# Kernel tuning notes

Hardware: AMD Instinct MI355X
Metric: run time of the kernel (lower is better)

The kernel has to match this reference:

```python
import jax, jax.numpy as jnp
import numpy as np

PATCH = 8      # patch_size
NFREQ = 8      # fourie_freq


def _fourier_feats(nH, nW, F, dtype):
    # Per-patch positional Fourier features: sin/cos of normalized patch-center
    # coords at F dyadic frequencies for both axes -> [nH, nW, 4F].
    iy = (jnp.arange(nH, dtype=jnp.float32) + 0.5) / nH
    ix = (jnp.arange(nW, dtype=jnp.float32) + 0.5) / nW
    freqs = (2.0 ** jnp.arange(F, dtype=jnp.float32)) * jnp.pi
    fy = iy[:, None] * freqs[None, :]  # [nH, F]
    fx = ix[:, None] * freqs[None, :]  # [nW, F]
    feats = jnp.concatenate([
        jnp.broadcast_to(jnp.sin(fy)[:, None, :], (nH, nW, F)),
        jnp.broadcast_to(jnp.cos(fy)[:, None, :], (nH, nW, F)),
        jnp.broadcast_to(jnp.sin(fx)[None, :, :], (nH, nW, F)),
        jnp.broadcast_to(jnp.cos(fx)[None, :, :], (nH, nW, F)),
    ], axis=-1)
    return feats.astype(dtype)


def setup_inputs() -> dict:
    key = jax.random.key(0)
    ks = jax.random.split(key, 5)
    B, C, H, W = 16, 64, 128, 128
    E, OC, P, F = 8, 64, PATCH, NFREQ
    GC = C + 4 * F  # gate_channel = 96
    x = jax.random.normal(ks[0], (B, C, H, W), jnp.float32)
    expert_w = jax.random.normal(ks[1], (E, OC, C, 3, 3), jnp.float32) * 0.05
    expert_b = jax.random.normal(ks[2], (E, OC), jnp.float32) * 0.05
    gate_w = jax.random.normal(ks[3], (E, GC * P * P), jnp.float32) * 0.02
    gate_b = jnp.zeros((E,), jnp.float32)
    return {"x": x, "expert_w": expert_w, "expert_b": expert_b,
            "gate_w": gate_w, "gate_b": gate_b}


def reference(x, expert_w, expert_b, gate_w, gate_b):
    B, C, H, W = x.shape
    E, OC = expert_w.shape[0], expert_w.shape[1]
    P, F = PATCH, NFREQ
    nH, nW = H // P, W // P

    # --- gating: per-patch softmax over experts ---
    # patches: [B, nH, nW, C, P, P] (matches nn.Flatten over (C,P,P))
    patches = x.reshape(B, C, nH, P, nW, P).transpose(0, 2, 4, 1, 3, 5)
    feats = _fourier_feats(nH, nW, F, x.dtype)                       # [nH,nW,4F]
    pos = jnp.broadcast_to(feats[None, :, :, :, None, None],
                           (B, nH, nW, 4 * F, P, P))
    gate_in = jnp.concatenate([patches, pos], axis=3).reshape(B, nH, nW, -1)
    logits = jnp.einsum('bhwf,ef->bhwe', gate_in, gate_w) + gate_b
    gate = jax.nn.softmax(logits, axis=-1)                           # [B,nH,nW,E]

    # --- experts: all E convs fused into a single conv, then gated combine ---
    wk = expert_w.reshape(E * OC, C, 3, 3)
    y = jax.lax.conv_general_dilated(
        x, wk, window_strides=(1, 1), padding='SAME',
        dimension_numbers=('NCHW', 'OIHW', 'NCHW'))
    y = y + expert_b.reshape(E * OC)[None, :, None, None]
    y = jax.nn.relu(y).reshape(B, E, OC, H, W)

    # upsample per-patch gates to pixel resolution: [B,E,H,W]
    g = gate.transpose(0, 3, 1, 2)                                   # [B,E,nH,nW]
    g = jnp.repeat(jnp.repeat(g, P, axis=2), P, axis=3)
    out = jnp.einsum('behw,bechw->bchw', g, y)                       # [B,OC,H,W]
    return out
```

## Files before the change

### kernel.cpp

```cpp
#include <hip/hip_runtime.h>

typedef short v8s __attribute__((ext_vector_type(8)));
typedef float v4f __attribute__((ext_vector_type(4)));

#define NCH    64
#define NHH    128
#define NWW    128
#define NOC    64
#define KSTEPS 18

#define CSTR 72
#define COLS 66
#define SLAB_BYTES (6 * COLS * CSTR * 2)
#define BBUF_OFF   SLAB_BYTES
#define LDSG_OFF   (SLAB_BYTES + 16384)
#define SMEM_BYTES 73728

#define GW_STRIDE 6144

__device__ __forceinline__ unsigned short f2bf(float f) {
  unsigned int u = __float_as_uint(f);
  u += 0x7FFFu + ((u >> 16) & 1u);
  return (unsigned short)(u >> 16);
}

__global__ void pack_b_kernel(const float* __restrict__ ew,
                              unsigned short* __restrict__ bp) {
  int f = blockIdx.x * 256 + threadIdx.x;
  int j = f & 7;
  int t = f >> 3;
  int lane = t & 63;
  t >>= 6;
  int nt = t & 3;
  t >>= 2;
  int s = t % KSTEPS;
  int e = t / KSTEPS;
  int k = s * 32 + (lane >> 4) * 8 + j;
  int n = nt * 16 + (lane & 15);
  int khw = k >> 6;
  int c = k & 63;
  bp[f] = f2bf(ew[((e * NOC + n) * NCH + c) * 9 + khw]);
}

__global__ __launch_bounds__(512) void gate_kernel(
    const float* __restrict__ x,
    const float* __restrict__ gw,
    const float* __restrict__ gb,
    float* __restrict__ gate_out) {
  __shared__ float xs[16][8][132];
  __shared__ float wsum[8][32];
  __shared__ float lg[16][8];

  const int pid = blockIdx.x;
  const int ph = pid & 15;
  const int b = pid >> 4;
  const int tid = threadIdx.x;
  const int e = tid >> 6;
  const int lane = tid & 63;

  if (tid < 256) {
    int e2 = tid >> 5, j = tid & 31;
    const float* p = gw + e2 * GW_STRIDE + 4096 + j * 64;
    float s = 0.f;
#pragma unroll
    for (int g = 0; g < 16; ++g) {
      float4 v = *(const float4*)(p + g * 4);
      s += v.x + v.y + v.z + v.w;
    }
    wsum[e2][j] = s;
  }

  float acc[16];
#pragma unroll
  for (int pw = 0; pw < 16; ++pw) acc[pw] = 0.f;

  const float* xrow = x + ((size_t)(b * NCH) * NHH + ph * 8) * NWW;

  for (int cc = 0; cc < 4; ++cc) {
    __syncthreads();
    for (int i = tid; i < 4096; i += 512) {
      int c = i >> 8;
      int py = (i >> 5) & 7;
      int w4 = i & 31;
      float4 v = *(const float4*)&xrow[(cc * 16 + c) * (NHH * NWW) + py * NWW + w4 * 4];
      *(float4*)&xs[c][py][w4 * 4] = v;
    }
    __syncthreads();
#pragma unroll
    for (int i = 0; i < 4; ++i) {
      int g = lane + 64 * i;
      int pxg = g & 1;
      int py = (g >> 1) & 7;
      int c = g >> 4;
      const float4 wv = *(const float4*)&gw[e * GW_STRIDE + (cc * 16 + c) * 64 + py * 8 + pxg * 4];
      const float* xp = &xs[c][py][pxg * 4];
#pragma unroll
      for (int pw = 0; pw < 16; ++pw) {
        float4 xv = *(const float4*)(xp + pw * 8);
        acc[pw] += xv.x * wv.x + xv.y * wv.y + xv.z * wv.z + xv.w * wv.w;
      }
    }
  }

#pragma unroll
  for (int pw = 0; pw < 16; ++pw) {
    float v = acc[pw];
#pragma unroll
    for (int off = 32; off > 0; off >>= 1) v += __shfl_xor(v, off, 64);
    if (lane == 0) lg[pw][e] = v;
  }
  __syncthreads();

  if (tid < 16) {
    const int pw = tid;
    const float cy = (ph + 0.5f) / 16.0f;
    const float cx = (pw + 0.5f) / 16.0f;
    float l[8];
#pragma unroll
    for (int ee = 0; ee < 8; ++ee) l[ee] = lg[pw][ee] + gb[ee];
    for (int j = 0; j < 32; ++j) {
      float freq = (float)(1 << (j & 7)) * 3.14159265358979323846f;
      float base = (j < 16) ? cy : cx;
      float a = base * freq;
      float v = ((j >> 3) & 1) ? cosf(a) : sinf(a);
#pragma unroll
      for (int ee = 0; ee < 8; ++ee) l[ee] += v * wsum[ee][j];
    }
    float mx = -1e30f;
#pragma unroll
    for (int ee = 0; ee < 8; ++ee) mx = fmaxf(mx, l[ee]);
    float sum = 0.f;
#pragma unroll
    for (int ee = 0; ee < 8; ++ee) { l[ee] = expf(l[ee] - mx); sum += l[ee]; }
    float inv = 1.0f / sum;
#pragma unroll
    for (int ee = 0; ee < 8; ++ee)
      gate_out[(pid * 16 + pw) * 8 + ee] = l[ee] * inv;
  }
}

__device__ __forceinline__ void load_stage(const unsigned short* __restrict__ bp,
                                           char* smem, int gs, int buf,
                                           int wid, int lane) {
  const char* gsrc = (const char*)bp + gs * 8192 + wid * 2048 + lane * 16;
  char* ldst = smem + BBUF_OFF + buf * 8192 + wid * 2048;
  __builtin_amdgcn_global_load_lds(
      (const __attribute__((address_space(1))) void*)gsrc,
      (__attribute__((address_space(3))) void*)ldst, 16, 0, 0);
  __builtin_amdgcn_global_load_lds(
      (const __attribute__((address_space(1))) void*)(gsrc + 1024),
      (__attribute__((address_space(3))) void*)(ldst + 1024), 16, 0, 0);
}

__global__ __launch_bounds__(256, 2) void moe_conv_kernel(
    const float* __restrict__ x,
    const float* __restrict__ eb,
    const unsigned short* __restrict__ bp,
    const float* __restrict__ gate,
    float* __restrict__ out) {
  __shared__ __align__(16) char smem[SMEM_BYTES];
  unsigned short* slab = (unsigned short*)smem;
  unsigned short* bbufs = (unsigned short*)(smem + BBUF_OFF);
  float* ldsg = (float*)(smem + LDSG_OFF);

  const int tid = threadIdx.x;
  const int bid = blockIdx.x;
  const int wseg = bid & 1;
  const int hq = (bid >> 1) & 31;
  const int b = bid >> 6;
  const int w0 = wseg * 64;
  const int wid = tid >> 6;
  const int lane = tid & 63;
  const int quad = lane >> 4;
  const int l15 = lane & 15;
  const int rp  = wid >> 1;
  const int och = wid & 1;
  const int ntb = och * 2;

  load_stage(bp, smem, 0, 0, wid, lane);

  if (tid < 64) {
    ldsg[tid] = gate[((b * 16 + (hq >> 1)) * 16 + wseg * 8 + (tid >> 3)) * 8 + (tid & 7)];
  }

  const int hbase = hq * 4 - 1;
  const int wbase = w0 - 1;
  for (int flat = tid; flat < 6 * 32 * COLS; flat += 256) {
    int col = flat % COLS;
    int t = flat / COLS;
    int cp = t & 31;
    int r = t >> 5;
    int gh = hbase + r;
    int gw_ = wbase + col;
    float v0 = 0.f, v1 = 0.f;
    if (((unsigned)gh < 128u) && ((unsigned)gw_ < 128u)) {
      const float* px = x + (((b * NCH + cp * 2) * NHH + gh) * NWW + gw_);
      v0 = px[0];
      v1 = px[NHH * NWW];
    }
    unsigned int pk = (unsigned int)f2bf(v0) | ((unsigned int)f2bf(v1) << 16);
    *(unsigned int*)&slab[(r * COLS + col) * CSTR + cp * 2] = pk;
  }
  __syncthreads();

  const v4f vzero = {0.f, 0.f, 0.f, 0.f};
  v4f oacc[8][2];
#pragma unroll
  for (int mt = 0; mt < 8; ++mt) {
    oacc[mt][0] = vzero;
    oacc[mt][1] = vzero;
  }

  const unsigned short* abase = &slab[(rp * 2 * COLS + l15) * CSTR + quad * 8];

  for (int e = 0; e < 8; ++e) {
    v4f vacc[8][2];
#pragma unroll
    for (int mt = 0; mt < 8; ++mt) {
      vacc[mt][0] = vzero;
      vacc[mt][1] = vzero;
    }

#pragma unroll
    for (int st = 0; st < 9; ++st) {
      const int gs = e * 9 + st;
      if (gs > 0) __syncthreads();
      if (gs + 1 < 72) load_stage(bp, smem, gs + 1, (gs + 1) & 1, wid, lane);

      const unsigned short* bstage = bbufs + (gs & 1) * 4096;
#pragma unroll
      for (int sub = 0; sub < 2; ++sub) {
        const int sl = st * 2 + sub;
        const int kh = sl / 6;
        const int kw = (sl / 2) % 3;
        const int ch = sl & 1;
        const v8s b0 = *(const v8s*)(bstage + (sub * 4 + ntb) * 512 + lane * 8);
        const v8s b1 = *(const v8s*)(bstage + (sub * 4 + ntb + 1) * 512 + lane * 8);
#pragma unroll
        for (int mt = 0; mt < 8; ++mt) {
          const v8s a = *(const v8s*)(abase +
              (((mt >> 2) + kh) * COLS + (mt & 3) * 16 + kw) * CSTR + ch * 32);
          vacc[mt][0] = __builtin_amdgcn_mfma_f32_16x16x32_bf16(a, b0, vacc[mt][0], 0, 0, 0);
          vacc[mt][1] = __builtin_amdgcn_mfma_f32_16x16x32_bf16(a, b1, vacc[mt][1], 0, 0, 0);
        }
      }
    }

    float bias0 = eb[e * NOC + ntb * 16 + l15];
    float bias1 = eb[e * NOC + (ntb + 1) * 16 + l15];
#pragma unroll
    for (int mt = 0; mt < 8; ++mt) {
      float g = ldsg[((mt & 3) * 2 + (quad >> 1)) * 8 + e];
#pragma unroll
      for (int r = 0; r < 4; ++r) {
        float v0 = fmaxf(vacc[mt][0][r] + bias0, 0.f);
        float v1 = fmaxf(vacc[mt][1][r] + bias1, 0.f);
        oacc[mt][0][r] += v0 * g;
        oacc[mt][1][r] += v1 * g;
      }
    }
  }

  __syncthreads();
  float* tb = (float*)smem + wid * 4352;
#pragma unroll
  for (int i = 0; i < 2; ++i)
#pragma unroll
    for (int mt = 0; mt < 8; ++mt)
      *(v4f*)(tb + (mt >> 2) * 2176 + (i * 16 + l15) * 68 + (mt & 3) * 16 + quad * 4) =
          oacc[mt][i];

  const int h0 = hq * 4 + rp * 2;
#pragma unroll
  for (int r2 = 0; r2 < 2; ++r2) {
    const int h = h0 + r2;
#pragma unroll
    for (int g4 = 0; g4 < 8; ++g4) {
      const int ocl = g4 * 4 + quad;
      const v4f vv = *(const v4f*)(tb + r2 * 2176 + ocl * 68 + l15 * 4);
      float* dst = out + ((b * NOC + och * 32 + ocl) * NHH + h) * NWW + w0 + l15 * 4;
      *(v4f*)dst = vv;
    }
  }
}

extern "C" void kernel_launch(void* const* d_in, const int* in_sizes, int n_in,
                              void* d_out, int out_size, void* d_ws, size_t ws_size,
                              hipStream_t stream) {
  const float* x  = (const float*)d_in[0];
  const float* ew = (const float*)d_in[1];
  const float* eb = (const float*)d_in[2];
  const float* gw = (const float*)d_in[3];
  const float* gb = (const float*)d_in[4];
  float* out = (float*)d_out;

  unsigned short* bp = (unsigned short*)d_ws;
  float* gate = (float*)((char*)d_ws + 589824);

  hipLaunchKernelGGL(pack_b_kernel, dim3(1152), dim3(256), 0, stream, ew, bp);
  hipLaunchKernelGGL(gate_kernel, dim3(256), dim3(512), 0, stream, x, gw, gb, gate);
  hipLaunchKernelGGL(moe_conv_kernel, dim3(1024), dim3(256), 0, stream, x, eb, bp, gate, out);
}
```

Before: 284.4 us.

## Load expert weights directly from global memory, dropping LDS double-buffer and barriers

Removes the double-buffered LDS staging of packed expert weights (global_load_lds plus a __syncthreads per stage). Each wave now reads its B fragments straight from global memory (L2/L1 cached) inside the k-loop, and MFMA sections are wrapped in s_setprio. This is meant to remove 72 block barriers and cut LDS use, which might raise occupancy, at the cost of exposing global load latency inside the inner loop.

```diff
diff --git a/kernel.cpp b/kernel.cpp
--- a/kernel.cpp
+++ b/kernel.cpp
@@ -12,9 +12,8 @@
 #define CSTR 72
 #define COLS 66
 #define SLAB_BYTES (6 * COLS * CSTR * 2)
-#define BBUF_OFF   SLAB_BYTES
-#define LDSG_OFF   (SLAB_BYTES + 16384)
-#define SMEM_BYTES 73728
+#define LDSG_OFF   69632
+#define SMEM_BYTES 70144
 
 #define GW_STRIDE 6144
 
@@ -139,19 +138,6 @@
   }
 }
 
-__device__ __forceinline__ void load_stage(const unsigned short* __restrict__ bp,
-                                           char* smem, int gs, int buf,
-                                           int wid, int lane) {
-  const char* gsrc = (const char*)bp + gs * 8192 + wid * 2048 + lane * 16;
-  char* ldst = smem + BBUF_OFF + buf * 8192 + wid * 2048;
-  __builtin_amdgcn_global_load_lds(
-      (const __attribute__((address_space(1))) void*)gsrc,
-      (__attribute__((address_space(3))) void*)ldst, 16, 0, 0);
-  __builtin_amdgcn_global_load_lds(
-      (const __attribute__((address_space(1))) void*)(gsrc + 1024),
-      (__attribute__((address_space(3))) void*)(ldst + 1024), 16, 0, 0);
-}
-
 __global__ __launch_bounds__(256, 2) void moe_conv_kernel(
     const float* __restrict__ x,
     const float* __restrict__ eb,
@@ -160,7 +146,6 @@
     float* __restrict__ out) {
   __shared__ __align__(16) char smem[SMEM_BYTES];
   unsigned short* slab = (unsigned short*)smem;
-  unsigned short* bbufs = (unsigned short*)(smem + BBUF_OFF);
   float* ldsg = (float*)(smem + LDSG_OFF);
 
   const int tid = threadIdx.x;
@@ -176,8 +161,6 @@
   const int rp  = wid >> 1;
   const int och = wid & 1;
   const int ntb = och * 2;
-
-  load_stage(bp, smem, 0, 0, wid, lane);
 
   if (tid < 64) {
     ldsg[tid] = gate[((b * 16 + (hq >> 1)) * 16 + wseg * 8 + (tid >> 3)) * 8 + (tid & 7)];
@@ -212,6 +195,7 @@
   }
 
   const unsigned short* abase = &slab[(rp * 2 * COLS + l15) * CSTR + quad * 8];
+  const unsigned short* bbase = bp + ntb * 512 + lane * 8;
 
   for (int e = 0; e < 8; ++e) {
     v4f vacc[8][2];
@@ -222,28 +206,22 @@
     }
 
 #pragma unroll
-    for (int st = 0; st < 9; ++st) {
-      const int gs = e * 9 + st;
-      if (gs > 0) __syncthreads();
-      if (gs + 1 < 72) load_stage(bp, smem, gs + 1, (gs + 1) & 1, wid, lane);
-
-      const unsigned short* bstage = bbufs + (gs & 1) * 4096;
-#pragma unroll
-      for (int sub = 0; sub < 2; ++sub) {
-        const int sl = st * 2 + sub;
-        const int kh = sl / 6;
-        const int kw = (sl / 2) % 3;
-        const int ch = sl & 1;
-        const v8s b0 = *(const v8s*)(bstage + (sub * 4 + ntb) * 512 + lane * 8);
-        const v8s b1 = *(const v8s*)(bstage + (sub * 4 + ntb + 1) * 512 + lane * 8);
-#pragma unroll
-        for (int mt = 0; mt < 8; ++mt) {
-          const v8s a = *(const v8s*)(abase +
-              (((mt >> 2) + kh) * COLS + (mt & 3) * 16 + kw) * CSTR + ch * 32);
-          vacc[mt][0] = __builtin_amdgcn_mfma_f32_16x16x32_bf16(a, b0, vacc[mt][0], 0, 0, 0);
-          vacc[mt][1] = __builtin_amdgcn_mfma_f32_16x16x32_bf16(a, b1, vacc[mt][1], 0, 0, 0);
-        }
+    for (int sl = 0; sl < KSTEPS; ++sl) {
+      const int kh = sl / 6;
+      const int kw = (sl / 2) % 3;
+      const int ch = sl & 1;
+      const unsigned short* bsrc = bbase + (e * KSTEPS + sl) * 2048;
+      const v8s b0 = *(const v8s*)(bsrc);
+      const v8s b1 = *(const v8s*)(bsrc + 512);
+      __builtin_amdgcn_s_setprio(1);
+#pragma unroll
+      for (int mt = 0; mt < 8; ++mt) {
+        const v8s a = *(const v8s*)(abase +
+            (((mt >> 2) + kh) * COLS + (mt & 3) * 16 + kw) * CSTR + ch * 32);
+        vacc[mt][0] = __builtin_amdgcn_mfma_f32_16x16x32_bf16(a, b0, vacc[mt][0], 0, 0, 0);
+        vacc[mt][1] = __builtin_amdgcn_mfma_f32_16x16x32_bf16(a, b1, vacc[mt][1], 0, 0, 0);
       }
+      __builtin_amdgcn_s_setprio(0);
     }
 
     float bias0 = eb[e * NOC + ntb * 16 + l15];
```

After: 772.9 us. 172% more time.

## Process expert pairs per K-step to reuse A fragments across two experts

Applied to the files above, without the earlier changes.

Reorders the packed weight layout so each K-stage holds the same K-slice for two experts. The main loop now handles two experts at once, loading each A fragment from LDS once and feeding it to four MFMAs instead of two. This halves A-operand LDS reads per MFMA. It also wraps the MFMA block in s_setprio. The cost is double the accumulator registers (64 more VGPRs/AGPRs), which may reduce occupancy or cause spills.

```diff
diff --git a/kernel.cpp b/kernel.cpp
--- a/kernel.cpp
+++ b/kernel.cpp
@@ -33,9 +33,12 @@
   t >>= 6;
   int nt = t & 3;
   t >>= 2;
-  int s = t % KSTEPS;
-  int e = t / KSTEPS;
-  int k = s * 32 + (lane >> 4) * 8 + j;
+  int e01 = t & 1;
+  int gs = t >> 1;
+  int sl = gs % KSTEPS;
+  int ep = gs / KSTEPS;
+  int e = ep * 2 + e01;
+  int k = sl * 32 + (lane >> 4) * 8 + j;
   int n = nt * 16 + (lane & 15);
   int khw = k >> 6;
   int c = k & 63;
@@ -213,50 +216,56 @@
 
   const unsigned short* abase = &slab[(rp * 2 * COLS + l15) * CSTR + quad * 8];
 
-  for (int e = 0; e < 8; ++e) {
-    v4f vacc[8][2];
+  for (int ep = 0; ep < 4; ++ep) {
+    v4f vacc[2][8][2];
 #pragma unroll
     for (int mt = 0; mt < 8; ++mt) {
-      vacc[mt][0] = vzero;
-      vacc[mt][1] = vzero;
-    }
-
-#pragma unroll
-    for (int st = 0; st < 9; ++st) {
-      const int gs = e * 9 + st;
+      vacc[0][mt][0] = vzero; vacc[0][mt][1] = vzero;
+      vacc[1][mt][0] = vzero; vacc[1][mt][1] = vzero;
+    }
+
+#pragma unroll
+    for (int sl = 0; sl < KSTEPS; ++sl) {
+      const int gs = ep * KSTEPS + sl;
       if (gs > 0) __syncthreads();
       if (gs + 1 < 72) load_stage(bp, smem, gs + 1, (gs + 1) & 1, wid, lane);
 
       const unsigned short* bstage = bbufs + (gs & 1) * 4096;
-#pragma unroll
-      for (int sub = 0; sub < 2; ++sub) {
-        const int sl = st * 2 + sub;
-        const int kh = sl / 6;
-        const int kw = (sl / 2) % 3;
-        const int ch = sl & 1;
-        const v8s b0 = *(const v8s*)(bstage + (sub * 4 + ntb) * 512 + lane * 8);
-        const v8s b1 = *(const v8s*)(bstage + (sub * 4 + ntb + 1) * 512 + lane * 8);
-#pragma unroll
-        for (int mt = 0; mt < 8; ++mt) {
-          const v8s a = *(const v8s*)(abase +
-              (((mt >> 2) + kh) * COLS + (mt & 3) * 16 + kw) * CSTR + ch * 32);
-          vacc[mt][0] = __builtin_amdgcn_mfma_f32_16x16x32_bf16(a, b0, vacc[mt][0], 0, 0, 0);
-          vacc[mt][1] = __builtin_amdgcn_mfma_f32_16x16x32_bf16(a, b1, vacc[mt][1], 0, 0, 0);
+      const int kh = sl / 6;
+      const int kw = (sl / 2) % 3;
+      const int ch = sl & 1;
+      const v8s b00 = *(const v8s*)(bstage + (ntb) * 512 + lane * 8);
+      const v8s b01 = *(const v8s*)(bstage + (ntb + 1) * 512 + lane * 8);
+      const v8s b10 = *(const v8s*)(bstage + (4 + ntb) * 512 + lane * 8);
+      const v8s b11 = *(const v8s*)(bstage + (4 + ntb + 1) * 512 + lane * 8);
+      __builtin_amdgcn_s_setprio(1);
+#pragma unroll
+      for (int mt = 0; mt < 8; ++mt) {
+        const v8s a = *(const v8s*)(abase +
+            (((mt >> 2) + kh) * COLS + (mt & 3) * 16 + kw) * CSTR + ch * 32);
+        vacc[0][mt][0] = __builtin_amdgcn_mfma_f32_16x16x32_bf16(a, b00, vacc[0][mt][0], 0, 0, 0);
+        vacc[0][mt][1] = __builtin_amdgcn_mfma_f32_16x16x32_bf16(a, b01, vacc[0][mt][1], 0, 0, 0);
+        vacc[1][mt][0] = __builtin_amdgcn_mfma_f32_16x16x32_bf16(a, b10, vacc[1][mt][0], 0, 0, 0);
+        vacc[1][mt][1] = __builtin_amdgcn_mfma_f32_16x16x32_bf16(a, b11, vacc[1][mt][1], 0, 0, 0);
+      }
+      __builtin_amdgcn_s_setprio(0);
+    }
+
+#pragma unroll
+    for (int e01 = 0; e01 < 2; ++e01) {
+      const int e = ep * 2 + e01;
+      float bias0 = eb[e * NOC + ntb * 16 + l15];
+      float bias1 = eb[e * NOC + (ntb + 1) * 16 + l15];
+#pragma unroll
+      for (int mt = 0; mt < 8; ++mt) {
+        float g = ldsg[((mt & 3) * 2 + (quad >> 1)) * 8 + e];
+#pragma unroll
+        for (int r = 0; r < 4; ++r) {
+          float v0 = fmaxf(vacc[e01][mt][0][r] + bias0, 0.f);
+          float v1 = fmaxf(vacc[e01][mt][1][r] + bias1, 0.f);
+          oacc[mt][0][r] += v0 * g;
+          oacc[mt][1][r] += v1 * g;
         }
-      }
-    }
-
-    float bias0 = eb[e * NOC + ntb * 16 + l15];
-    float bias1 = eb[e * NOC + (ntb + 1) * 16 + l15];
-#pragma unroll
-    for (int mt = 0; mt < 8; ++mt) {
-      float g = ldsg[((mt & 3) * 2 + (quad >> 1)) * 8 + e];
-#pragma unroll
-      for (int r = 0; r < 4; ++r) {
-        float v0 = fmaxf(vacc[mt][0][r] + bias0, 0.f);
-        float v1 = fmaxf(vacc[mt][1][r] + bias1, 0.f);
-        oacc[mt][0][r] += v0 * g;
-        oacc[mt][1][r] += v1 * g;
       }
     }
   }
```

After: 293.3 us. 1.03x slower.

## Triple-buffer weight stages, swizzle input slab, remap waves to full-OC rows

Applied to the files above, without the earlier changes.

Weight staging moves from double to triple buffering with prefetch two stages ahead. The full __syncthreads is replaced by a vmcnt wait plus a raw barrier. The input slab gets an XOR-style rotation swizzle to avoid LDS bank conflicts on A-fragment reads. Each wave now handles one output row across all 64 output channels (4x4 MFMA tiles) instead of two rows by 32 channels, so each A fragment is reused across four B tiles. MFMA blocks also run under raised s_setprio. This adds LDS use for the third buffer and relies on exact vmcnt accounting, which may be fragile if load_stage issues a different number of loads.

```diff
diff --git a/kernel.cpp b/kernel.cpp
--- a/kernel.cpp
+++ b/kernel.cpp
@@ -13,8 +13,9 @@
 #define COLS 66
 #define SLAB_BYTES (6 * COLS * CSTR * 2)
 #define BBUF_OFF   SLAB_BYTES
-#define LDSG_OFF   (SLAB_BYTES + 16384)
-#define SMEM_BYTES 73728
+#define NBUF 3
+#define LDSG_OFF   (SLAB_BYTES + NBUF * 8192)
+#define SMEM_BYTES (LDSG_OFF + 256)
 
 #define GW_STRIDE 6144
 
@@ -173,9 +174,6 @@
   const int lane = tid & 63;
   const int quad = lane >> 4;
   const int l15 = lane & 15;
-  const int rp  = wid >> 1;
-  const int och = wid & 1;
-  const int ntb = och * 2;
 
   load_stage(bp, smem, 0, 0, wid, lane);
 
@@ -199,88 +197,103 @@
       v1 = px[NHH * NWW];
     }
     unsigned int pk = (unsigned int)f2bf(v0) | ((unsigned int)f2bf(v1) << 16);
-    *(unsigned int*)&slab[(r * COLS + col) * CSTR + cp * 2] = pk;
-  }
+    int srow = r * COLS + col;
+    int boff = ((cp * 4) + ((srow & 7) << 4)) & 127;
+    *(unsigned int*)((char*)slab + srow * 144 + boff) = pk;
+  }
+
+  load_stage(bp, smem, 1, 1, wid, lane);
   __syncthreads();
 
   const v4f vzero = {0.f, 0.f, 0.f, 0.f};
-  v4f oacc[8][2];
-#pragma unroll
-  for (int mt = 0; mt < 8; ++mt) {
-    oacc[mt][0] = vzero;
-    oacc[mt][1] = vzero;
-  }
-
-  const unsigned short* abase = &slab[(rp * 2 * COLS + l15) * CSTR + quad * 8];
+  v4f oacc[4][4];
+#pragma unroll
+  for (int mt = 0; mt < 4; ++mt)
+#pragma unroll
+    for (int nt = 0; nt < 4; ++nt) oacc[mt][nt] = vzero;
+
+  const int q16 = quad * 16;
+  const int lw  = l15 + 2 * wid;
+  const int rowb = (wid * COLS + l15) * 144;
 
   for (int e = 0; e < 8; ++e) {
-    v4f vacc[8][2];
-#pragma unroll
-    for (int mt = 0; mt < 8; ++mt) {
-      vacc[mt][0] = vzero;
-      vacc[mt][1] = vzero;
-    }
+    v4f vacc[4][4];
+#pragma unroll
+    for (int mt = 0; mt < 4; ++mt)
+#pragma unroll
+      for (int nt = 0; nt < 4; ++nt) vacc[mt][nt] = vzero;
 
 #pragma unroll
     for (int st = 0; st < 9; ++st) {
       const int gs = e * 9 + st;
-      if (gs > 0) __syncthreads();
-      if (gs + 1 < 72) load_stage(bp, smem, gs + 1, (gs + 1) & 1, wid, lane);
-
-      const unsigned short* bstage = bbufs + (gs & 1) * 4096;
+      if (gs > 0) {
+        asm volatile("s_waitcnt vmcnt(2)" ::: "memory");
+        __builtin_amdgcn_s_barrier();
+        __builtin_amdgcn_sched_barrier(0);
+      }
+      {
+        const int g2 = gs + 2;
+        const int gsrc = (g2 < 72) ? g2 : 71;
+        load_stage(bp, smem, gsrc, (st + 2) % 3, wid, lane);
+      }
+
+      const unsigned short* bstage = bbufs + (st % 3) * 4096;
 #pragma unroll
       for (int sub = 0; sub < 2; ++sub) {
         const int sl = st * 2 + sub;
         const int kh = sl / 6;
         const int kw = (sl / 2) % 3;
         const int ch = sl & 1;
-        const v8s b0 = *(const v8s*)(bstage + (sub * 4 + ntb) * 512 + lane * 8);
-        const v8s b1 = *(const v8s*)(bstage + (sub * 4 + ntb + 1) * 512 + lane * 8);
-#pragma unroll
-        for (int mt = 0; mt < 8; ++mt) {
-          const v8s a = *(const v8s*)(abase +
-              (((mt >> 2) + kh) * COLS + (mt & 3) * 16 + kw) * CSTR + ch * 32);
-          vacc[mt][0] = __builtin_amdgcn_mfma_f32_16x16x32_bf16(a, b0, vacc[mt][0], 0, 0, 0);
-          vacc[mt][1] = __builtin_amdgcn_mfma_f32_16x16x32_bf16(a, b1, vacc[mt][1], 0, 0, 0);
+        v8s bf[4];
+#pragma unroll
+        for (int nt = 0; nt < 4; ++nt)
+          bf[nt] = *(const v8s*)(bstage + (sub * 4 + nt) * 512 + lane * 8);
+        const int rot = ((lw + 2 * kh + kw) & 7) << 4;
+        const int aoff = (q16 + ch * 64 + rot) & 127;
+        const char* arow = (const char*)slab + rowb + (kh * COLS + kw) * 144 + aoff;
+        __builtin_amdgcn_s_setprio(1);
+#pragma unroll
+        for (int mt = 0; mt < 4; ++mt) {
+          const v8s a = *(const v8s*)(arow + mt * 2304);
+#pragma unroll
+          for (int nt = 0; nt < 4; ++nt)
+            vacc[mt][nt] = __builtin_amdgcn_mfma_f32_16x16x32_bf16(a, bf[nt], vacc[mt][nt], 0, 0, 0);
         }
+        __builtin_amdgcn_s_setprio(0);
       }
     }
 
-    float bias0 = eb[e * NOC + ntb * 16 + l15];
-    float bias1 = eb[e * NOC + (ntb + 1) * 16 + l15];
-#pragma unroll
-    for (int mt = 0; mt < 8; ++mt) {
-      float g = ldsg[((mt & 3) * 2 + (quad >> 1)) * 8 + e];
-#pragma unroll
-      for (int r = 0; r < 4; ++r) {
-        float v0 = fmaxf(vacc[mt][0][r] + bias0, 0.f);
-        float v1 = fmaxf(vacc[mt][1][r] + bias1, 0.f);
-        oacc[mt][0][r] += v0 * g;
-        oacc[mt][1][r] += v1 * g;
-      }
+    float bias[4];
+#pragma unroll
+    for (int nt = 0; nt < 4; ++nt) bias[nt] = eb[e * NOC + nt * 16 + l15];
+#pragma unroll
+    for (int mt = 0; mt < 4; ++mt) {
+      float g = ldsg[(mt * 2 + (quad >> 1)) * 8 + e];
+#pragma unroll
+      for (int nt = 0; nt < 4; ++nt)
+#pragma unroll
+        for (int r = 0; r < 4; ++r) {
+          float v = fmaxf(vacc[mt][nt][r] + bias[nt], 0.f);
+          oacc[mt][nt][r] += v * g;
+        }
     }
   }
 
   __syncthreads();
   float* tb = (float*)smem + wid * 4352;
 #pragma unroll
-  for (int i = 0; i < 2; ++i)
-#pragma unroll
-    for (int mt = 0; mt < 8; ++mt)
-      *(v4f*)(tb + (mt >> 2) * 2176 + (i * 16 + l15) * 68 + (mt & 3) * 16 + quad * 4) =
-          oacc[mt][i];
-
-  const int h0 = hq * 4 + rp * 2;
-#pragma unroll
-  for (int r2 = 0; r2 < 2; ++r2) {
-    const int h = h0 + r2;
-#pragma unroll
-    for (int g4 = 0; g4 < 8; ++g4) {
-      const int ocl = g4 * 4 + quad;
-      const v4f vv = *(const v4f*)(tb + r2 * 2176 + ocl * 68 + l15 * 4);
-      float* dst = out + ((b * NOC + och * 32 + ocl) * NHH + h) * NWW + w0 + l15 * 4;
-      *(v4f*)dst = vv;
-    }
+  for (int mt = 0; mt < 4; ++mt)
+#pragma unroll
+    for (int nt = 0; nt < 4; ++nt)
+      *(v4f*)(tb + (nt * 16 + l15) * 68 + mt * 16 + quad * 4) = oacc[mt][nt];
+
+  const int h = hq * 4 + wid;
+#pragma unroll
+  for (int g4 = 0; g4 < 16; ++g4) {
+    const int ocl = g4 * 4 + quad;
+    const v4f vv = *(const v4f*)(tb + ocl * 68 + l15 * 4);
+    float* dst = out + ((b * NOC + ocl) * NHH + h) * NWW + w0 + l15 * 4;
+    *(v4f*)dst = vv;
   }
 }
 
```

After: 276.0 us. 3.0% less time.
